# Kernel tuning notes

Hardware: AMD Instinct MI355X
Metric: run time of the kernel (lower is better)

The kernel has to match this reference:

```python
import jax, jax.numpy as jnp
import numpy as np

MIN_NORM = 1e-15
N = 10000        # num_nodes
E = 320000       # num edges (avg degree 32)
F_IN = 512       # in_features
HID = 256        # hardcoded encoder hidden dim
D_HYP = 2        # Poincare embedding dim
HEIGHT = 2
MAX_SIZE = 0.999
MIN_SCALE = HEIGHT * (MAX_SIZE / (HEIGHT + 1))  # = 0.666, scale clamp lower bound
MAX_SCALE = MAX_SIZE


def setup_inputs() -> dict:
    key = jax.random.key(0)
    ks = jax.random.split(key, 5)
    feature = jax.random.normal(ks[0], (N, F_IN), jnp.float32)
    edge_index = jax.random.randint(ks[1], (2, E), 0, N, dtype=jnp.int64)
    W1 = jax.random.normal(ks[2], (F_IN, HID), jnp.float32) / np.sqrt(F_IN).astype(np.float32)
    b1 = jnp.zeros((HID,), jnp.float32)
    W2 = jax.random.normal(ks[3], (HID, D_HYP), jnp.float32) / np.sqrt(HID).astype(np.float32)
    b2 = jnp.zeros((D_HYP,), jnp.float32)
    scale = jnp.ones((1,), jnp.float32)  # init_size overridden to 1.0 in __init__
    return {"feature": feature, "edge_index": edge_index, "W1": W1, "b1": b1,
            "W2": W2, "b2": b2, "scale": scale}


def _gcn_agg(h, src, dst):
    # symmetric-normalized edge_index gather/aggregate (message passing)
    deg = jax.ops.segment_sum(jnp.ones((src.shape[0],), h.dtype), dst, num_segments=N)
    deg = jnp.maximum(deg, 1.0)
    norm = jax.lax.rsqrt(deg[src] * deg[dst])            # [E]
    msg = h[src] * norm[:, None]                          # [E, C] gather (irregular)
    return jax.ops.segment_sum(msg, dst, num_segments=N)  # [N, C] scatter-add


def reference(feature, edge_index, W1, b1, W2, b2, scale):
    src, dst = edge_index[0], edge_index[1]
    # 2-layer graph encoder (linear -> aggregate -> relu, linear -> aggregate)
    h = jax.nn.relu(_gcn_agg(feature @ W1 + b1, src, dst))   # [N, HID]
    u = _gcn_agg(h @ W2 + b2, src, dst)                      # [N, D_HYP] tangent at origin
    # lift to Lorentz model (k=-1) via expmap0: x = [cosh|u|, sinh|u| * u/|u|]
    un = jnp.maximum(jnp.linalg.norm(u, axis=-1, keepdims=True), MIN_NORM)
    x_l = jnp.concatenate([jnp.cosh(un), jnp.sinh(un) * u / un], axis=-1)  # [N, D_HYP+1]
    # Lorentz -> Poincare: p = x_space / (1 + x_time)
    p = x_l[:, 1:] / (1.0 + x_l[:, :1])
    # normalize: F.normalize(p, dim=-1) * scale.clamp(min_size, max_size)
    pn = jnp.maximum(jnp.linalg.norm(p, axis=-1, keepdims=True), 1e-12)
    s = jnp.clip(scale, MIN_SCALE, MAX_SCALE)
    p = p / pn * s
    # project onto Poincare ball of curvature k=-1 with eps=MIN_NORM
    norm = jnp.maximum(jnp.linalg.norm(p, axis=-1, keepdims=True), MIN_NORM)
    maxnorm = 1.0 - MIN_NORM
    return jnp.where(norm > maxnorm, p / norm * maxnorm, p)
```

## Files before the change

kernel.cpp:

```cpp
#include <hip/hip_runtime.h>
#include <math.h>

#define N_NODES 10000
#define N_EDGES 320000
#define F_IN 512
#define HID 256
#define PAD_DEG 80
#define N_GEMM_BLKS 157
#define BUILD_BLKS ((N_EDGES + 255) / 256)

typedef _Float16 half8 __attribute__((ext_vector_type(8)));
typedef float floatx4 __attribute__((ext_vector_type(4)));

__device__ __forceinline__ void fma4(float4& acc, float s, const float4& v) {
    acc.x += s * v.x; acc.y += s * v.y; acc.z += s * v.z; acc.w += s * v.w;
}


__global__ __launch_bounds__(256) void k_pre(const float* __restrict__ W1,
                                             int* __restrict__ count,
                                             _Float16* __restrict__ Bt_hi,
                                             _Float16* __restrict__ Bt_lo) {
    int i = blockIdx.x * blockDim.x + threadIdx.x;
    if (i < 10240) count[i] = 0;
    int k = i >> 8, n = i & 255;
    float v = W1[i];
    _Float16 hi = (_Float16)v;
    Bt_hi[n * F_IN + k] = hi;
    Bt_lo[n * F_IN + k] = (_Float16)(v - (float)hi);
}


__global__ __launch_bounds__(256) void k_main(const float* __restrict__ A,
                                              const _Float16* __restrict__ Bt_hi,
                                              const _Float16* __restrict__ Bt_lo,
                                              const float* __restrict__ b1,
                                              float* __restrict__ h0,
                                              const int* __restrict__ ei,
                                              int* __restrict__ count,
                                              int* __restrict__ csr) {
    const int tid = threadIdx.x;

    if (blockIdx.x >= N_GEMM_BLKS) {
        int e = (blockIdx.x - N_GEMM_BLKS) * 256 + tid;
        if (e < N_EDGES) {
            int src = ei[e];
            int dst = ei[N_EDGES + e];
            int pos = atomicAdd(&count[dst], 1);
            csr[dst * PAD_DEG + pos] = src;
        }
        return;
    }

    const int lane = tid & 63, w = tid >> 6;
    const int quad = lane >> 4, l15 = lane & 15;
    const int row0 = blockIdx.x * 64;
    const int colw = w * 64;
    floatx4 acc[4][4] = {};

    const float*    aptr[4];
    const _Float16* bhptr[4];
    const _Float16* blptr[4];
    #pragma unroll
    for (int mi = 0; mi < 4; ++mi) {
        int ar = row0 + mi * 16 + l15;
        if (ar >= N_NODES) ar = N_NODES - 1;
        aptr[mi] = A + (size_t)ar * F_IN + quad * 8;
    }
    #pragma unroll
    for (int ni = 0; ni < 4; ++ni) {
        int col = colw + ni * 16 + l15;
        bhptr[ni] = Bt_hi + (size_t)col * F_IN + quad * 8;
        blptr[ni] = Bt_lo + (size_t)col * F_IN + quad * 8;
    }

    float4 apf[4][2];
    half8  bhp[4], blp[4];
    #pragma unroll
    for (int mi = 0; mi < 4; ++mi) {
        apf[mi][0] = *(const float4*)(aptr[mi]);
        apf[mi][1] = *(const float4*)(aptr[mi] + 4);
    }
    #pragma unroll
    for (int ni = 0; ni < 4; ++ni) {
        bhp[ni] = *(const half8*)(bhptr[ni]);
        blp[ni] = *(const half8*)(blptr[ni]);
    }

    #pragma unroll
    for (int kk = 0; kk < 16; ++kk) {
        half8 ah[4], al[4];
        #pragma unroll
        for (int mi = 0; mi < 4; ++mi) {
            float av[8] = {apf[mi][0].x, apf[mi][0].y, apf[mi][0].z, apf[mi][0].w,
                           apf[mi][1].x, apf[mi][1].y, apf[mi][1].z, apf[mi][1].w};
            #pragma unroll
            for (int j = 0; j < 8; ++j) {
                _Float16 h = (_Float16)av[j];
                ah[mi][j] = h;
                al[mi][j] = (_Float16)(av[j] - (float)h);
            }
        }
        if (kk < 15) {
            const int k1 = (kk + 1) * 32;
            #pragma unroll
            for (int mi = 0; mi < 4; ++mi) {
                apf[mi][0] = *(const float4*)(aptr[mi] + k1);
                apf[mi][1] = *(const float4*)(aptr[mi] + k1 + 4);
            }
        }
        #pragma unroll
        for (int ni = 0; ni < 4; ++ni)
            #pragma unroll
            for (int mi = 0; mi < 4; ++mi) {
                acc[mi][ni] = __builtin_amdgcn_mfma_f32_16x16x32_f16(ah[mi], bhp[ni], acc[mi][ni], 0, 0, 0);
                acc[mi][ni] = __builtin_amdgcn_mfma_f32_16x16x32_f16(ah[mi], blp[ni], acc[mi][ni], 0, 0, 0);
                acc[mi][ni] = __builtin_amdgcn_mfma_f32_16x16x32_f16(al[mi], bhp[ni], acc[mi][ni], 0, 0, 0);
            }
        if (kk < 15) {
            const int k1 = (kk + 1) * 32;
            #pragma unroll
            for (int ni = 0; ni < 4; ++ni) {
                bhp[ni] = *(const half8*)(bhptr[ni] + k1);
                blp[ni] = *(const half8*)(blptr[ni] + k1);
            }
        }
    }

    #pragma unroll
    for (int mi = 0; mi < 4; ++mi)
        #pragma unroll
        for (int ni = 0; ni < 4; ++ni) {
            int colb = colw + ni * 16 + l15;
            float bias = b1[colb];
            #pragma unroll
            for (int reg = 0; reg < 4; ++reg) {
                int rowb = row0 + mi * 16 + quad * 4 + reg;
                if (rowb < N_NODES) h0[(size_t)rowb * HID + colb] = acc[mi][ni][reg] + bias;
            }
        }
}


__global__ __launch_bounds__(256) void k_agg1(const float* __restrict__ h0,
                                              const int* __restrict__ csr,
                                              const int* __restrict__ count,
                                              const float* __restrict__ W2,
                                              const float* __restrict__ b2,
                                              float* __restrict__ u0) {
    __shared__ int2 nb[4][PAD_DEG];
    const int wid = threadIdx.x >> 6;
    const int lane = threadIdx.x & 63;
    const int n = blockIdx.x * 4 + wid;
    const int deg = count[n];
    const float degd = (float)(deg > 0 ? deg : 1);
    const int* row = csr + (size_t)n * PAD_DEG;
    for (int j = lane; j < deg; j += 64) {
        int s = row[j];
        int cs = count[s];
        float wq = rsqrtf((float)(cs > 0 ? cs : 1) * degd);
        nb[wid][j] = make_int2(s, __float_as_int(wq));
    }
    __syncthreads();

    const int off = lane << 2;
    float4 acc0 = {0,0,0,0}, acc1 = {0,0,0,0}, acc2 = {0,0,0,0}, acc3 = {0,0,0,0};
    int j = 0;
    for (; j + 16 <= deg; j += 16) {
        int2 e[16];
        #pragma unroll
        for (int q = 0; q < 16; ++q) e[q] = nb[wid][j + q];
        float4 v[16];
        #pragma unroll
        for (int q = 0; q < 16; ++q)
            v[q] = *(const float4*)(h0 + ((size_t)e[q].x << 8) + off);
        #pragma unroll
        for (int q = 0; q < 16; q += 4) {
            fma4(acc0, __int_as_float(e[q + 0].y), v[q + 0]);
            fma4(acc1, __int_as_float(e[q + 1].y), v[q + 1]);
            fma4(acc2, __int_as_float(e[q + 2].y), v[q + 2]);
            fma4(acc3, __int_as_float(e[q + 3].y), v[q + 3]);
        }
    }
    for (; j + 4 <= deg; j += 4) {
        int2 e0 = nb[wid][j+0], e1 = nb[wid][j+1], e2 = nb[wid][j+2], e3 = nb[wid][j+3];
        float4 v0 = *(const float4*)(h0 + ((size_t)e0.x << 8) + off);
        float4 v1 = *(const float4*)(h0 + ((size_t)e1.x << 8) + off);
        float4 v2 = *(const float4*)(h0 + ((size_t)e2.x << 8) + off);
        float4 v3 = *(const float4*)(h0 + ((size_t)e3.x << 8) + off);
        fma4(acc0, __int_as_float(e0.y), v0);
        fma4(acc1, __int_as_float(e1.y), v1);
        fma4(acc2, __int_as_float(e2.y), v2);
        fma4(acc3, __int_as_float(e3.y), v3);
    }
    for (; j < deg; ++j) {
        int2 e = nb[wid][j];
        float4 v = *(const float4*)(h0 + ((size_t)e.x << 8) + off);
        fma4(acc0, __int_as_float(e.y), v);
    }
    acc0.x += acc1.x + acc2.x + acc3.x;
    acc0.y += acc1.y + acc2.y + acc3.y;
    acc0.z += acc1.z + acc2.z + acc3.z;
    acc0.w += acc1.w + acc2.w + acc3.w;
    acc0.x = fmaxf(acc0.x, 0.f); acc0.y = fmaxf(acc0.y, 0.f);
    acc0.z = fmaxf(acc0.z, 0.f); acc0.w = fmaxf(acc0.w, 0.f);
    float4 wa = *(const float4*)(W2 + (lane << 3));
    float4 wb = *(const float4*)(W2 + (lane << 3) + 4);
    float p0 = acc0.x * wa.x + acc0.y * wa.z + acc0.z * wb.x + acc0.w * wb.z;
    float p1 = acc0.x * wa.y + acc0.y * wa.w + acc0.z * wb.y + acc0.w * wb.w;
    #pragma unroll
    for (int o = 32; o > 0; o >>= 1) {
        p0 += __shfl_down(p0, o);
        p1 += __shfl_down(p1, o);
    }
    if (lane == 0) {
        u0[2 * n]     = p0 + b2[0];
        u0[2 * n + 1] = p1 + b2[1];
    }
}


__global__ __launch_bounds__(256) void k_agg2(const float* __restrict__ u0,
                                              const int* __restrict__ csr,
                                              const int* __restrict__ count,
                                              const float* __restrict__ scale,
                                              float* __restrict__ out) {
    int n = blockIdx.x * 4 + (threadIdx.x >> 6);
    int lane = threadIdx.x & 63;
    if (n >= N_NODES) return;
    int deg = count[n];
    float degd = (float)(deg > 0 ? deg : 1);
    const int* row = csr + (size_t)n * PAD_DEG;
    float a0 = 0.f, a1 = 0.f;
    for (int j = lane; j < deg; j += 64) {
        int s = row[j];
        int cs = count[s];
        float wq = rsqrtf((float)(cs > 0 ? cs : 1) * degd);
        float2 uv = *(const float2*)(u0 + 2 * (size_t)s);
        a0 += wq * uv.x;
        a1 += wq * uv.y;
    }
    #pragma unroll
    for (int o = 32; o > 0; o >>= 1) {
        a0 += __shfl_down(a0, o);
        a1 += __shfl_down(a1, o);
    }
    if (lane == 0) {
        float un = fmaxf(sqrtf(a0 * a0 + a1 * a1), 1e-15f);
        float t = tanhf(0.5f * un) / un;
        float p0 = a0 * t, p1 = a1 * t;
        float pn = fmaxf(sqrtf(p0 * p0 + p1 * p1), 1e-12f);
        float s = fminf(fmaxf(scale[0], 0.666f), 0.999f);
        p0 = p0 / pn * s; p1 = p1 / pn * s;
        float nn = fmaxf(sqrtf(p0 * p0 + p1 * p1), 1e-15f);
        if (nn > 1.0f) { p0 = p0 / nn; p1 = p1 / nn; }
        out[2 * n]     = p0;
        out[2 * n + 1] = p1;
    }
}


extern "C" void kernel_launch(void* const* d_in, const int* in_sizes, int n_in,
                              void* d_out, int out_size, void* d_ws, size_t ws_size,
                              hipStream_t stream) {
    const float* feature = (const float*)d_in[0];
    const int*   ei      = (const int*)d_in[1];
    const float* W1      = (const float*)d_in[2];
    const float* b1      = (const float*)d_in[3];
    const float* W2      = (const float*)d_in[4];
    const float* b2      = (const float*)d_in[5];
    const float* scale   = (const float*)d_in[6];
    float* out = (float*)d_out;

    char* W = (char*)d_ws;
    int*      count = (int*)W;
    int*      csr   = (int*)(W + 40960);
    float*    h0    = (float*)(W + 3240960);
    float*    u0    = (float*)(W + 13480960);
    _Float16* Bt_hi = (_Float16*)(W + 13560960);
    _Float16* Bt_lo = (_Float16*)(W + 13823104);

    k_pre<<<dim3(512), dim3(256), 0, stream>>>(W1, count, Bt_hi, Bt_lo);
    k_main<<<dim3(N_GEMM_BLKS + BUILD_BLKS), dim3(256), 0, stream>>>(
        feature, Bt_hi, Bt_lo, b1, h0, ei, count, csr);
    k_agg1<<<dim3((N_NODES + 3) / 4), dim3(256), 0, stream>>>(h0, csr, count, W2, b2, u0);
    k_agg2<<<dim3((N_NODES + 3) / 4), dim3(256), 0, stream>>>(u0, csr, count, scale, out);
}
```

Measured before the change: 161.1 us.

## Stage GEMM tiles in LDS via direct global-to-LDS loads with double buffering

The first-layer GEMM now uses 64x64 output tiles across 632 blocks instead of 64x256 tiles across 157 blocks. A/B k-slices are loaded straight into XOR-swizzled shared memory with global_load_lds and double-buffered, so loads overlap compute and waves share staged data rather than each loading from global memory. Block indices are remapped to group tiles for cache locality. This adds a barrier per k-step and more blocks that each reload A for every column tile.

```diff
diff --git a/kernel.cpp b/kernel.cpp
--- a/kernel.cpp
+++ b/kernel.cpp
@@ -6,11 +6,18 @@
 #define F_IN 512
 #define HID 256
 #define PAD_DEG 80
-#define N_GEMM_BLKS 157
+#define N_GEMM_BLKS 632
 #define BUILD_BLKS ((N_EDGES + 255) / 256)
 
 typedef _Float16 half8 __attribute__((ext_vector_type(8)));
 typedef float floatx4 __attribute__((ext_vector_type(4)));
+
+typedef const __attribute__((address_space(1))) void* gas_ptr;
+typedef __attribute__((address_space(3))) void* las_ptr;
+
+__device__ __forceinline__ void dma16(const void* g, void* l) {
+    __builtin_amdgcn_global_load_lds((gas_ptr)g, (las_ptr)l, 16, 0, 0);
+}
 
 __device__ __forceinline__ void fma4(float4& acc, float s, const float4& v) {
     acc.x += s * v.x; acc.y += s * v.y; acc.z += s * v.z; acc.w += s * v.w;
@@ -39,6 +46,9 @@
                                               const int* __restrict__ ei,
                                               int* __restrict__ count,
                                               int* __restrict__ csr) {
+    __shared__ float    As[2][2048];
+    __shared__ _Float16 Bhs[2][2048];
+    __shared__ _Float16 Bls[2][2048];
     const int tid = threadIdx.x;
 
     if (blockIdx.x >= N_GEMM_BLKS) {
@@ -52,48 +62,70 @@
         return;
     }
 
+    const int b = blockIdx.x;
+    const int t = (b & 7) * 79 + (b >> 3);
+    const int row0 = (t >> 2) * 64, col0 = (t & 3) * 64;
+
+    const int sA0 = tid, sA1 = tid + 256;
+    const int rA0 = sA0 >> 3, hA0 = (sA0 & 7) ^ (rA0 & 7);
+    const int rA1 = sA1 >> 3, hA1 = (sA1 & 7) ^ (rA1 & 7);
+    int gr0 = row0 + rA0; if (gr0 > N_NODES - 1) gr0 = N_NODES - 1;
+    int gr1 = row0 + rA1; if (gr1 > N_NODES - 1) gr1 = N_NODES - 1;
+    const float* gA0 = A + (size_t)gr0 * F_IN + hA0 * 4;
+    const float* gA1 = A + (size_t)gr1 * F_IN + hA1 * 4;
+    const int cB = tid >> 2, hB = (tid & 3) ^ (cB & 3);
+    const _Float16* gBh = Bt_hi + (size_t)(col0 + cB) * F_IN + hB * 8;
+    const _Float16* gBl = Bt_lo + (size_t)(col0 + cB) * F_IN + hB * 8;
+
+    char* lA  = (char*)&As[0][0];
+    char* lBh = (char*)&Bhs[0][0];
+    char* lBl = (char*)&Bls[0][0];
+    const int dA0 = sA0 * 16, dA1 = sA1 * 16, dB = tid * 16;
+
+    dma16(gA0, lA + dA0);
+    dma16(gA1, lA + dA1);
+    dma16(gBh, lBh + dB);
+    dma16(gBl, lBl + dB);
+
     const int lane = tid & 63, w = tid >> 6;
     const int quad = lane >> 4, l15 = lane & 15;
-    const int row0 = blockIdx.x * 64;
-    const int colw = w * 64;
-    floatx4 acc[4][4] = {};
-
-    const float*    aptr[4];
-    const _Float16* bhptr[4];
-    const _Float16* blptr[4];
-    #pragma unroll
-    for (int mi = 0; mi < 4; ++mi) {
-        int ar = row0 + mi * 16 + l15;
-        if (ar >= N_NODES) ar = N_NODES - 1;
-        aptr[mi] = A + (size_t)ar * F_IN + quad * 8;
-    }
-    #pragma unroll
-    for (int ni = 0; ni < 4; ++ni) {
-        int col = colw + ni * 16 + l15;
-        bhptr[ni] = Bt_hi + (size_t)col * F_IN + quad * 8;
-        blptr[ni] = Bt_lo + (size_t)col * F_IN + quad * 8;
-    }
-
-    float4 apf[4][2];
-    half8  bhp[4], blp[4];
-    #pragma unroll
-    for (int mi = 0; mi < 4; ++mi) {
-        apf[mi][0] = *(const float4*)(aptr[mi]);
-        apf[mi][1] = *(const float4*)(aptr[mi] + 4);
-    }
-    #pragma unroll
-    for (int ni = 0; ni < 4; ++ni) {
-        bhp[ni] = *(const half8*)(bhptr[ni]);
-        blp[ni] = *(const half8*)(blptr[ni]);
-    }
-
-    #pragma unroll
-    for (int kk = 0; kk < 16; ++kk) {
-        half8 ah[4], al[4];
-        #pragma unroll
-        for (int mi = 0; mi < 4; ++mi) {
-            float av[8] = {apf[mi][0].x, apf[mi][0].y, apf[mi][0].z, apf[mi][0].w,
-                           apf[mi][1].x, apf[mi][1].y, apf[mi][1].z, apf[mi][1].w};
+    const int wm = (w >> 1) * 32, wn = (w & 1) * 32;
+    floatx4 acc[2][2] = {};
+
+    int aoff[2][2], boff[2];
+    #pragma unroll
+    for (int mi = 0; mi < 2; ++mi) {
+        int r = wm + mi * 16 + l15;
+        aoff[mi][0] = r * 128 + ((2 * quad)     ^ (r & 7)) * 16;
+        aoff[mi][1] = r * 128 + ((2 * quad + 1) ^ (r & 7)) * 16;
+    }
+    #pragma unroll
+    for (int ni = 0; ni < 2; ++ni) {
+        int n = wn + ni * 16 + l15;
+        boff[ni] = n * 64 + (quad ^ (n & 3)) * 16;
+    }
+
+    __syncthreads();
+
+    int buf = 0;
+    for (int it = 0; it < 16; ++it) {
+        if (it < 15) {
+            const int k1 = (it + 1) * 32;
+            const int nb = buf ^ 1;
+            dma16(gA0 + k1, lA  + nb * 8192 + dA0);
+            dma16(gA1 + k1, lA  + nb * 8192 + dA1);
+            dma16(gBh + k1, lBh + nb * 4096 + dB);
+            dma16(gBl + k1, lBl + nb * 4096 + dB);
+        }
+        const char* bA = lA  + buf * 8192;
+        const char* bH = lBh + buf * 4096;
+        const char* bL = lBl + buf * 4096;
+        half8 ah[2], al[2], bhf[2], blf[2];
+        #pragma unroll
+        for (int mi = 0; mi < 2; ++mi) {
+            float4 f0 = *(const float4*)(bA + aoff[mi][0]);
+            float4 f1 = *(const float4*)(bA + aoff[mi][1]);
+            float av[8] = {f0.x, f0.y, f0.z, f0.w, f1.x, f1.y, f1.z, f1.w};
             #pragma unroll
             for (int j = 0; j < 8; ++j) {
                 _Float16 h = (_Float16)av[j];
@@ -101,41 +133,32 @@
                 al[mi][j] = (_Float16)(av[j] - (float)h);
             }
         }
-        if (kk < 15) {
-            const int k1 = (kk + 1) * 32;
+        #pragma unroll
+        for (int ni = 0; ni < 2; ++ni) {
+            bhf[ni] = *(const half8*)(bH + boff[ni]);
+            blf[ni] = *(const half8*)(bL + boff[ni]);
+        }
+        #pragma unroll
+        for (int ni = 0; ni < 2; ++ni)
             #pragma unroll
-            for (int mi = 0; mi < 4; ++mi) {
-                apf[mi][0] = *(const float4*)(aptr[mi] + k1);
-                apf[mi][1] = *(const float4*)(aptr[mi] + k1 + 4);
+            for (int mi = 0; mi < 2; ++mi) {
+                acc[mi][ni] = __builtin_amdgcn_mfma_f32_16x16x32_f16(ah[mi], bhf[ni], acc[mi][ni], 0, 0, 0);
+                acc[mi][ni] = __builtin_amdgcn_mfma_f32_16x16x32_f16(ah[mi], blf[ni], acc[mi][ni], 0, 0, 0);
+                acc[mi][ni] = __builtin_amdgcn_mfma_f32_16x16x32_f16(al[mi], bhf[ni], acc[mi][ni], 0, 0, 0);
             }
-        }
-        #pragma unroll
-        for (int ni = 0; ni < 4; ++ni)
-            #pragma unroll
-            for (int mi = 0; mi < 4; ++mi) {
-                acc[mi][ni] = __builtin_amdgcn_mfma_f32_16x16x32_f16(ah[mi], bhp[ni], acc[mi][ni], 0, 0, 0);
-                acc[mi][ni] = __builtin_amdgcn_mfma_f32_16x16x32_f16(ah[mi], blp[ni], acc[mi][ni], 0, 0, 0);
-                acc[mi][ni] = __builtin_amdgcn_mfma_f32_16x16x32_f16(al[mi], bhp[ni], acc[mi][ni], 0, 0, 0);
-            }
-        if (kk < 15) {
-            const int k1 = (kk + 1) * 32;
-            #pragma unroll
-            for (int ni = 0; ni < 4; ++ni) {
-                bhp[ni] = *(const half8*)(bhptr[ni] + k1);
-                blp[ni] = *(const half8*)(blptr[ni] + k1);
-            }
-        }
-    }
-
-    #pragma unroll
-    for (int mi = 0; mi < 4; ++mi)
-        #pragma unroll
-        for (int ni = 0; ni < 4; ++ni) {
-            int colb = colw + ni * 16 + l15;
+        __syncthreads();
+        buf ^= 1;
+    }
+
+    #pragma unroll
+    for (int mi = 0; mi < 2; ++mi)
+        #pragma unroll
+        for (int ni = 0; ni < 2; ++ni) {
+            int colb = col0 + wn + ni * 16 + l15;
             float bias = b1[colb];
             #pragma unroll
             for (int reg = 0; reg < 4; ++reg) {
-                int rowb = row0 + mi * 16 + quad * 4 + reg;
+                int rowb = row0 + wm + mi * 16 + quad * 4 + reg;
                 if (rowb < N_NODES) h0[(size_t)rowb * HID + colb] = acc[mi][ni][reg] + bias;
             }
         }
```

Measured after the change: 150.8 us. -6.4%, faster.
